# Kernel optimization log

Measured on AMD Instinct MI355X. Metric: run time of the kernel, lower is better.

The kernel has to match this reference:

```python
import jax, jax.numpy as jnp
import numpy as np

NX = 320   # image matrix (nRead)
NC = 8     # coils
NT = 8     # motion states
M = 65536  # non-Cartesian k-space samples per frame
OS = 2     # gridding oversampling factor


def setup_inputs() -> dict:
    key = jax.random.key(0)
    ks = jax.random.split(key, 7)
    kspace_r = jax.random.normal(ks[0], (NC, M), jnp.float32)
    kspace_i = jax.random.normal(ks[1], (NC, M), jnp.float32)
    # k-space trajectory normalized to [-0.5, 0.5)
    traj = jax.random.uniform(ks[2], (M, 2, NT), jnp.float32, -0.5, 0.5)
    csm_r = jax.random.normal(ks[3], (NC, NX, NX), jnp.float32)
    csm_i = jax.random.normal(ks[4], (NC, NX, NX), jnp.float32)
    dcf = jax.random.uniform(ks[5], (M, NT), jnp.float32)
    # motion/flow field in pixels, [NX, NX, 2, NT]
    motions = 3.0 * jax.random.normal(ks[6], (NX, NX, 2, NT), jnp.float32)
    return dict(kspace_r=kspace_r, kspace_i=kspace_i, traj=traj,
                csm_r=csm_r, csm_i=csm_i, dcf=dcf, motions=motions)


def _grid_adjoint(kspace, traj_t, dcf_t, csm):
    """Adjoint NUFFT (gpuNUFFT adj_op): density-compensated bilinear gridding
    onto a 2x oversampled Cartesian grid, inverse FFT, center crop,
    deapodization, and conjugate coil combination."""
    G = OS * NX
    data = (kspace * dcf_t[None, :]).astype(jnp.complex64)  # [NC, M]
    u = (traj_t[:, 0] + 0.5) * G
    v = (traj_t[:, 1] + 0.5) * G
    u0 = jnp.floor(u)
    v0 = jnp.floor(v)
    du = (u - u0).astype(jnp.float32)
    dv = (v - v0).astype(jnp.float32)
    i0 = u0.astype(jnp.int32) % G
    i1 = (i0 + 1) % G
    j0 = v0.astype(jnp.int32) % G
    j1 = (j0 + 1) % G
    grid = jnp.zeros((NC, G, G), jnp.complex64)
    grid = grid.at[:, i0, j0].add(data * ((1.0 - du) * (1.0 - dv)))
    grid = grid.at[:, i1, j0].add(data * (du * (1.0 - dv)))
    grid = grid.at[:, i0, j1].add(data * ((1.0 - du) * dv))
    grid = grid.at[:, i1, j1].add(data * (du * dv))
    im_os = jnp.fft.fftshift(
        jnp.fft.ifft2(jnp.fft.ifftshift(grid, axes=(-2, -1)), axes=(-2, -1)),
        axes=(-2, -1))
    s = (G - NX) // 2
    im = im_os[:, s:s + NX, s:s + NX]  # [NC, NX, NX]
    # deapodization: FT of the triangle (bilinear) gridding kernel is sinc^2
    x = (jnp.arange(NX, dtype=jnp.float32) - NX // 2) / G
    d = jnp.sinc(x) ** 2
    im = im / (d[:, None] * d[None, :])
    # conjugate coil combine with sensitivity maps
    return jnp.sum(jnp.conj(csm) * im, axis=0).astype(jnp.complex64)


def _bilinear_warp(im, flow):
    """apply_sparse_motion: sparse bilinear-interpolation warp of a 2D image
    by a per-pixel displacement field flow[..., 0:2] (in pixels)."""
    Nx, Ny = im.shape
    xs = jnp.arange(Nx, dtype=jnp.float32)[:, None] + flow[..., 0]
    ys = jnp.arange(Ny, dtype=jnp.float32)[None, :] + flow[..., 1]
    xs = jnp.clip(xs, 0.0, Nx - 1.0)
    ys = jnp.clip(ys, 0.0, Ny - 1.0)
    x0 = jnp.floor(xs).astype(jnp.int32)
    y0 = jnp.floor(ys).astype(jnp.int32)
    x1 = jnp.minimum(x0 + 1, Nx - 1)
    y1 = jnp.minimum(y0 + 1, Ny - 1)
    dx = xs - x0.astype(jnp.float32)
    dy = ys - y0.astype(jnp.float32)
    return ((1.0 - dx) * (1.0 - dy) * im[x0, y0]
            + dx * (1.0 - dy) * im[x1, y0]
            + (1.0 - dx) * dy * im[x0, y1]
            + dx * dy * im[x1, y1])


def reference(kspace_r, kspace_i, traj, csm_r, csm_i, dcf, motions):
    kspace = (kspace_r + 1j * kspace_i).astype(jnp.complex64)
    csm = (csm_r + 1j * csm_i).astype(jnp.complex64)

    def frame(traj_t, dcf_t, flow_t):
        im = _grid_adjoint(kspace, traj_t, dcf_t, csm)
        return _bilinear_warp(im, flow_t)

    # vmap over motion states: traj[..., t], dcf[..., t], motions[..., t]
    per_frame = jax.vmap(frame, in_axes=(2, 1, 3))(traj, dcf, motions)  # [NT, NX, NX]
    out = jnp.sum(per_frame, axis=0)  # temporal sum, complex [NX, NX]
    return jnp.stack([out.real, out.imag], axis=-1)  # [NX, NX, 2]
```

## Files before the change

### kernel.cpp

```cpp
#include <hip/hip_runtime.h>
#include <math.h>

#define NXI 320
#define NCI 8
#define NTI 8
#define MI  65536
#define GI  640
#define G2I (GI*GI)
#define NPIX (NXI*NXI)
#define REC_F 20
#define SP 642
#define NBINS (NTI*G2I)
#define SCAN_BLKS (NBINS/1024)

__device__ inline float2 cmul(float2 a, float2 b) {
    return make_float2(a.x*b.x - a.y*b.y, a.x*b.y + a.y*b.x);
}
__device__ inline float2 cadd(float2 a, float2 b) { return make_float2(a.x+b.x, a.y+b.y); }
__device__ inline float2 csub(float2 a, float2 b) { return make_float2(a.x-b.x, a.y-b.y); }

__device__ inline float2 shfl_xor_c(float2 v, int m) {
    return make_float2(__shfl_xor(v.x, m, 64), __shfl_xor(v.y, m, 64));
}

__device__ inline void cell_of(const float* __restrict__ traj, int m, int f,
                               int& i0s, int& j0s, float& du, float& dv)
{
    float tu = traj[(m*2 + 0)*NTI + f];
    float tv = traj[(m*2 + 1)*NTI + f];
    float u = (tu + 0.5f) * (float)GI;
    float v = (tv + 0.5f) * (float)GI;
    float fu = floorf(u), fv = floorf(v);
    du = u - fu; dv = v - fv;
    i0s = (int)fu + GI/2; if (i0s >= GI) i0s -= GI;
    j0s = (int)fv + GI/2; if (j0s >= GI) j0s -= GI;
}

__global__ __launch_bounds__(256) void count_cells(
    const float* __restrict__ traj, int* __restrict__ counts)
{
    int tid = blockIdx.x * 256 + threadIdx.x;
    int f = tid >> 16, m = tid & (MI - 1);
    int i0s, j0s; float du, dv;
    cell_of(traj, m, f, i0s, j0s, du, dv);
    atomicAdd(&counts[f*G2I + i0s*GI + j0s], 1);
}

__device__ inline int scan1024(int v, int tid, int* tmp) {
    tmp[tid] = v; __syncthreads();
    for (int d = 1; d < 1024; d <<= 1) {
        int y = (tid >= d) ? tmp[tid - d] : 0;
        __syncthreads();
        tmp[tid] += y;
        __syncthreads();
    }
    return tmp[tid];
}

__global__ __launch_bounds__(1024) void scanA(const int* __restrict__ counts,
                                              int* __restrict__ binstart,
                                              int* __restrict__ sums)
{
    __shared__ int tmp[1024];
    int tid = threadIdx.x;
    int i = blockIdx.x * 1024 + tid;
    int v = counts[i];
    int incl = scan1024(v, tid, tmp);
    binstart[i] = incl - v;
    if (tid == 1023) sums[blockIdx.x] = incl;
}

__global__ __launch_bounds__(1024) void scanB(int* __restrict__ sums)
{
    __shared__ int tmp[1024];
    int tid = threadIdx.x;
    int base = tid * 4;
    int v[4]; int s = 0;
    #pragma unroll
    for (int q = 0; q < 4; ++q) {
        int idx = base + q;
        v[q] = (idx < SCAN_BLKS) ? sums[idx] : 0;
        s += v[q];
    }
    int incl = scan1024(s, tid, tmp);
    int run = incl - s;
    #pragma unroll
    for (int q = 0; q < 4; ++q) {
        int idx = base + q;
        if (idx < SCAN_BLKS) sums[idx] = run;
        run += v[q];
    }
}

__global__ __launch_bounds__(1024) void scanC(int* __restrict__ binstart,
                                              const int* __restrict__ sums,
                                              int* __restrict__ cursor)
{
    int i = blockIdx.x * 1024 + threadIdx.x;
    int v = binstart[i] + sums[blockIdx.x];
    binstart[i] = v;
    cursor[i] = v;
    if (i == NBINS - 1) binstart[NBINS] = NTI * MI;
}

__global__ __launch_bounds__(256) void scatter_cells(
    const float* __restrict__ kr, const float* __restrict__ ki,
    const float* __restrict__ traj, const float* __restrict__ dcf,
    int* __restrict__ cursor, float* __restrict__ recs)
{
    int tid = blockIdx.x * 256 + threadIdx.x;
    int f = tid >> 16, m = tid & (MI - 1);
    int i0s, j0s; float du, dv;
    cell_of(traj, m, f, i0s, j0s, du, dv);
    float w = dcf[m*NTI + f];
    int slot = atomicAdd(&cursor[f*G2I + i0s*GI + j0s], 1);
    float4* r = (float4*)(recs + (size_t)slot * REC_F);
    r[0] = make_float4(du, dv, 0.f, 0.f);
    #pragma unroll
    for (int q = 0; q < 4; ++q) {
        int c0 = 2*q;
        r[1+q] = make_float4(kr[c0*MI + m]*w,     ki[c0*MI + m]*w,
                             kr[(c0+1)*MI + m]*w, ki[(c0+1)*MI + m]*w);
    }
}

__device__ inline void dft5p(float2 x0, float2 x1, float2 x2, float2 x3, float2 x4,
                             float2* X)
{
    const float c1 = 0.309016994f, c2 = -0.809016994f;
    const float s1 = 0.951056516f, s2 =  0.587785252f;
    float2 S1 = cadd(x1, x4), D1 = csub(x1, x4);
    float2 S2 = cadd(x2, x3), D2 = csub(x2, x3);
    X[0] = make_float2(x0.x + S1.x + S2.x, x0.y + S1.y + S2.y);
    float2 A = make_float2(x0.x + c1*S1.x + c2*S2.x, x0.y + c1*S1.y + c2*S2.y);
    float2 T = make_float2(s1*D1.x + s2*D2.x,        s1*D1.y + s2*D2.y);
    float2 B = make_float2(x0.x + c2*S1.x + c1*S2.x, x0.y + c2*S1.y + c1*S2.y);
    float2 U = make_float2(s2*D1.x - s1*D2.x,        s2*D1.y - s1*D2.y);
    X[1] = make_float2(A.x - T.y, A.y + T.x);
    X[4] = make_float2(A.x + T.y, A.y - T.x);
    X[2] = make_float2(B.x - U.y, B.y + U.x);
    X[3] = make_float2(B.x + U.y, B.y - U.x);
}

__device__ inline int fft640_reg(float2* a, int lane, float2* Z,
                                 const float2* __restrict__ T)
{
    const float PI = 3.14159265358979f;
    #pragma unroll
    for (int s = 0; s < 6; ++s) {
        const int h = 32 >> s;
        bool low = (lane & h) == 0;
        float2 wt = T[(lane << s) & 63];
        float2 w = low ? make_float2(1.f, 0.f) : wt;
        #pragma unroll
        for (int n = 0; n < 10; ++n) {
            float2 p = shfl_xor_c(a[n], h);
            float2 t = low ? cadd(p, a[n]) : csub(a[n], p);
            a[n] = cmul(t, w);
        }
    }
    int k1 = __brev(lane) >> 26;
    float th = (2.0f * PI / 640.0f) * (float)k1;
    float sn, cs;
    __sincosf(th, &sn, &cs);
    float2 wb = make_float2(cs, sn);
    float2 w = wb;
    #pragma unroll
    for (int n = 1; n < 10; ++n) {
        a[n] = cmul(a[n], w);
        w = cmul(w, wb);
    }
    float2 E[5], O[5];
    dft5p(a[0], a[2], a[4], a[6], a[8], E);
    dft5p(a[1], a[3], a[5], a[7], a[9], O);
    const float2 tk[5] = {{1.f, 0.f},
                          { 0.809016994f, 0.587785252f},
                          { 0.309016994f, 0.951056516f},
                          {-0.309016994f, 0.951056516f},
                          {-0.809016994f, 0.587785252f}};
    #pragma unroll
    for (int k = 0; k < 5; ++k) {
        float2 t = cmul(tk[k], O[k]);
        Z[k]     = cadd(E[k], t);
        Z[k + 5] = csub(E[k], t);
    }
    return k1;
}

__device__ inline void fill_T(float2* T, int tid, int nthr) {
    const float PI = 3.14159265358979f;
    for (int q = tid; q < 64; q += nthr) {
        float sn, cs;
        __sincosf((2.0f * PI / 64.0f) * q, &sn, &cs);
        T[q] = make_float2(cs, sn);
    }
}

__global__ __launch_bounds__(512) void row_fft(
    const int* __restrict__ binstart, const float* __restrict__ recs,
    float2* __restrict__ rowout)
{
    __shared__ float2 A[NCI][SP];
    __shared__ int boff[2][GI+1];
    __shared__ float2 T[64];
    int bid = blockIdx.x;
    int i = bid % GI;
    int f = bid / GI;
    int tid = threadIdx.x;
    fill_T(&T[0], tid, 512);
    int im1 = i ? i - 1 : GI - 1;
    const int base0 = f*G2I + i*GI;
    const int base1 = f*G2I + im1*GI;
    for (int k = tid; k <= GI; k += 512) {
        boff[0][k] = binstart[base0 + k];
        boff[1][k] = binstart[base1 + k];
    }
    __syncthreads();

    for (int j = tid; j < GI; j += 512) {
        int jm1 = j ? j - 1 : GI - 1;
        float2 acc[NCI];
        #pragma unroll
        for (int c = 0; c < NCI; ++c) acc[c] = make_float2(0.f, 0.f);
        #pragma unroll
        for (int p = 0; p < 2; ++p) {
            #pragma unroll
            for (int side = 0; side < 2; ++side) {
                int b = side ? jm1 : j;
                int s0 = boff[p][b], s1 = boff[p][b+1];
                for (int s = s0; s < s1; ++s) {
                    const float4* R = (const float4*)(recs + (size_t)s*REC_F);
                    float4 h4 = R[0];
                    float wr = p ? h4.x : (1.f - h4.x);
                    float w  = wr * (side ? h4.y : (1.f - h4.y));
                    float4 d0 = R[1], d1 = R[2], d2 = R[3], d3 = R[4];
                    acc[0].x += w*d0.x; acc[0].y += w*d0.y;
                    acc[1].x += w*d0.z; acc[1].y += w*d0.w;
                    acc[2].x += w*d1.x; acc[2].y += w*d1.y;
                    acc[3].x += w*d1.z; acc[3].y += w*d1.w;
                    acc[4].x += w*d2.x; acc[4].y += w*d2.y;
                    acc[5].x += w*d2.z; acc[5].y += w*d2.w;
                    acc[6].x += w*d3.x; acc[6].y += w*d3.y;
                    acc[7].x += w*d3.z; acc[7].y += w*d3.w;
                }
            }
        }
        #pragma unroll
        for (int c = 0; c < NCI; ++c) A[c][j] = acc[c];
    }
    __syncthreads();

    int wv = tid >> 6, lane = tid & 63;
    float2 a[10];
    #pragma unroll
    for (int n = 0; n < 10; ++n) a[n] = A[wv][10*lane + n];
    float2 Z[10];
    int k1 = fft640_reg(a, lane, Z, &T[0]);
    #pragma unroll
    for (int k2 = 0; k2 < 10; ++k2) {
        int yc = k1 + 64*k2 + 160; if (yc >= GI) yc -= GI;
        A[wv][yc] = Z[k2];
    }
    float2* dst = rowout + (((size_t)f*NCI + wv)*GI + i)*NXI;
    #pragma unroll
    for (int q = 0; q < 5; ++q) {
        int yc = lane + 64*q;
        dst[yc] = A[wv][yc];
    }
}

__global__ __launch_bounds__(512) void col_fft(
    const float2* __restrict__ rowout, float2* __restrict__ colimg)
{
    __shared__ float2 A[8][SP];
    __shared__ float2 T[64];
    int bid = blockIdx.x;
    int g = bid % 40;
    int c = (bid / 40) % NCI;
    int f = bid / (40*NCI);
    int y0 = g * 8;
    int tid = threadIdx.x;
    fill_T(&T[0], tid, 512);
    const float2* src = rowout + ((size_t)f*NCI + c)*GI*NXI + y0;
    for (int idx = tid; idx < 8*GI; idx += 512) {
        int l = idx & 7, k = idx >> 3;
        A[l][k] = src[(size_t)k*NXI + l];
    }
    __syncthreads();
    int wv = tid >> 6, lane = tid & 63;
    float2 a[10];
    #pragma unroll
    for (int n = 0; n < 10; ++n) a[n] = A[wv][10*lane + n];
    float2 Z[10];
    int k1 = fft640_reg(a, lane, Z, &T[0]);
    #pragma unroll
    for (int k2 = 0; k2 < 10; ++k2) {
        int xx = k1 + 64*k2 + 160; if (xx >= GI) xx -= GI;
        A[wv][xx] = Z[k2];
    }
    __syncthreads();
    float2* dst = colimg + ((size_t)f*NCI + c)*NPIX + y0;
    for (int idx = tid; idx < 8*NXI; idx += 512) {
        int l = idx & 7, xx = idx >> 3;
        dst[(size_t)xx*NXI + l] = A[l][xx];
    }
}

__global__ __launch_bounds__(256) void combine_kernel(
    const float2* __restrict__ colimg, const float* __restrict__ csr,
    const float* __restrict__ csi, float2* __restrict__ img)
{
    int f = blockIdx.y;
    int pix = blockIdx.x * 256 + threadIdx.x;
    int x = pix / NXI, y = pix - x*NXI;
    const float PI = 3.14159265358979f;
    float tx = (x - 160) * (1.0f/GI);
    float ty = (y - 160) * (1.0f/GI);
    float dx = 1.0f, dy = 1.0f;
    if (x != 160) { float s = __sinf(PI*tx) / (PI*tx); dx = s*s; }
    if (y != 160) { float s = __sinf(PI*ty) / (PI*ty); dy = s*s; }
    float scale = 1.0f / ((float)G2I * dx * dy);
    float accr = 0.f, acci = 0.f;
    #pragma unroll
    for (int c = 0; c < NCI; ++c) {
        float2 g = colimg[((size_t)f*NCI + c)*NPIX + pix];
        float cr = csr[c*NPIX + pix];
        float ci = csi[c*NPIX + pix];
        accr += cr*g.x + ci*g.y;
        acci += cr*g.y - ci*g.x;
    }
    img[(size_t)f*NPIX + pix] = make_float2(accr*scale, acci*scale);
}

__global__ __launch_bounds__(256) void warp_sum(
    const float2* __restrict__ img, const float* __restrict__ motions,
    float* __restrict__ out)
{
    int pix = blockIdx.x * 256 + threadIdx.x;
    int x = pix / NXI, y = pix - x*NXI;
    float accr = 0.f, acci = 0.f;
    #pragma unroll
    for (int f = 0; f < NTI; ++f) {
        float fx = motions[(size_t)(pix*2 + 0)*NTI + f];
        float fy = motions[(size_t)(pix*2 + 1)*NTI + f];
        float xs = fminf(fmaxf((float)x + fx, 0.0f), (float)(NXI-1));
        float ys = fminf(fmaxf((float)y + fy, 0.0f), (float)(NXI-1));
        int x0 = (int)floorf(xs);
        int y0 = (int)floorf(ys);
        int x1 = min(x0+1, NXI-1);
        int y1 = min(y0+1, NXI-1);
        float dx = xs - (float)x0;
        float dy = ys - (float)y0;
        const float2* im = img + (size_t)f*NPIX;
        float2 v00 = im[x0*NXI + y0];
        float2 v10 = im[x1*NXI + y0];
        float2 v01 = im[x0*NXI + y1];
        float2 v11 = im[x1*NXI + y1];
        float w00 = (1.f-dx)*(1.f-dy), w10 = dx*(1.f-dy);
        float w01 = (1.f-dx)*dy,       w11 = dx*dy;
        accr += w00*v00.x + w10*v10.x + w01*v01.x + w11*v11.x;
        acci += w00*v00.y + w10*v10.y + w01*v01.y + w11*v11.y;
    }
    out[pix*2+0] = accr;
    out[pix*2+1] = acci;
}

extern "C" void kernel_launch(void* const* d_in, const int* in_sizes, int n_in,
                              void* d_out, int out_size, void* d_ws, size_t ws_size,
                              hipStream_t stream)
{
    const float* kr   = (const float*)d_in[0];
    const float* ki   = (const float*)d_in[1];
    const float* traj = (const float*)d_in[2];
    const float* csr  = (const float*)d_in[3];
    const float* csi  = (const float*)d_in[4];
    const float* dcf  = (const float*)d_in[5];
    const float* mot  = (const float*)d_in[6];
    float* out = (float*)d_out;

    char* ws = (char*)d_ws;
    float*  recs     = (float*)ws;
    ws += (size_t)NTI * MI * REC_F * sizeof(float);
    float2* rowout   = (float2*)ws;
    ws += (size_t)NTI * NCI * GI * NXI * sizeof(float2);
    float2* colimg   = (float2*)ws;
    ws += (size_t)NTI * NCI * NPIX * sizeof(float2);
    float2* img      = (float2*)ws;
    ws += (size_t)NTI * NPIX * sizeof(float2);
    int*    counts   = (int*)ws;  ws += (size_t)NBINS * sizeof(int);
    int*    binstart = (int*)ws;  ws += ((size_t)NBINS + 16) * sizeof(int);
    int*    cursor   = (int*)ws;  ws += (size_t)NBINS * sizeof(int);
    int*    sums     = (int*)ws;  ws += (size_t)SCAN_BLKS * sizeof(int);

    hipMemsetAsync(counts, 0, (size_t)NBINS * sizeof(int), stream);
    count_cells  <<<NTI*MI/256, 256, 0, stream>>>(traj, counts);
    scanA        <<<SCAN_BLKS, 1024, 0, stream>>>(counts, binstart, sums);
    scanB        <<<1,         1024, 0, stream>>>(sums);
    scanC        <<<SCAN_BLKS, 1024, 0, stream>>>(binstart, sums, cursor);
    scatter_cells<<<NTI*MI/256, 256, 0, stream>>>(kr, ki, traj, dcf, cursor, recs);
    row_fft      <<<NTI*GI,     512, 0, stream>>>(binstart, recs, rowout);
    col_fft      <<<NTI*NCI*40, 512, 0, stream>>>(rowout, colimg);
    combine_kernel<<<dim3(NPIX/256, NTI), 256, 0, stream>>>(colimg, csr, csi, img);
    warp_sum     <<<NPIX/256,   256, 0, stream>>>(img, mot, out);
}
```

Baseline: 344.3 us.

## Vectorize complex math, prune FFT outputs, swizzle shared memory, merge gather loops

Rewrites the complex arithmetic with two-wide float vector types so the compiler can emit packed FP32 instructions. The 640-point FFT now computes and writes only the 320 cropped outputs and works out its twiddles with sincos instead of reading a shared table. The row gather reads bin offsets straight from global memory and walks two adjacent bins as one contiguous range. Column-FFT shared arrays use an XOR swizzle instead of padding to avoid bank conflicts, and launch bounds now request higher occupancy. The risks are extra transcendental instructions, uncached global reads of bin offsets, and register pressure under the tighter launch bounds.

```diff
diff --git a/kernel.cpp b/kernel.cpp
--- a/kernel.cpp
+++ b/kernel.cpp
@@ -9,18 +9,22 @@
 #define G2I (GI*GI)
 #define NPIX (NXI*NXI)
 #define REC_F 20
-#define SP 642
 #define NBINS (NTI*G2I)
 #define SCAN_BLKS (NBINS/1024)
 
-__device__ inline float2 cmul(float2 a, float2 b) {
-    return make_float2(a.x*b.x - a.y*b.y, a.x*b.y + a.y*b.x);
-}
-__device__ inline float2 cadd(float2 a, float2 b) { return make_float2(a.x+b.x, a.y+b.y); }
-__device__ inline float2 csub(float2 a, float2 b) { return make_float2(a.x-b.x, a.y-b.y); }
-
-__device__ inline float2 shfl_xor_c(float2 v, int m) {
-    return make_float2(__shfl_xor(v.x, m, 64), __shfl_xor(v.y, m, 64));
+typedef float v2f __attribute__((ext_vector_type(2)));
+
+__device__ inline v2f cmul(v2f a, v2f b) {
+    v2f axx = __builtin_shufflevector(a, a, 0, 0);
+    v2f ayy = __builtin_shufflevector(a, a, 1, 1);
+    v2f byx = __builtin_shufflevector(b, b, 1, 0);
+    v2f r = axx * b;
+    v2f t = ayy * byx;
+    return r + v2f{-t.x, t.y};
+}
+
+__device__ inline v2f shfl_xor_v(v2f v, int m) {
+    return v2f{__shfl_xor(v.x, m, 64), __shfl_xor(v.y, m, 64)};
 }
 
 __device__ inline void cell_of(const float* __restrict__ traj, int m, int f,
@@ -124,124 +128,123 @@
     }
 }
 
-__device__ inline void dft5p(float2 x0, float2 x1, float2 x2, float2 x3, float2 x4,
-                             float2* X)
+__device__ inline void dft5p(v2f x0, v2f x1, v2f x2, v2f x3, v2f x4, v2f* X)
 {
     const float c1 = 0.309016994f, c2 = -0.809016994f;
     const float s1 = 0.951056516f, s2 =  0.587785252f;
-    float2 S1 = cadd(x1, x4), D1 = csub(x1, x4);
-    float2 S2 = cadd(x2, x3), D2 = csub(x2, x3);
-    X[0] = make_float2(x0.x + S1.x + S2.x, x0.y + S1.y + S2.y);
-    float2 A = make_float2(x0.x + c1*S1.x + c2*S2.x, x0.y + c1*S1.y + c2*S2.y);
-    float2 T = make_float2(s1*D1.x + s2*D2.x,        s1*D1.y + s2*D2.y);
-    float2 B = make_float2(x0.x + c2*S1.x + c1*S2.x, x0.y + c2*S1.y + c1*S2.y);
-    float2 U = make_float2(s2*D1.x - s1*D2.x,        s2*D1.y - s1*D2.y);
-    X[1] = make_float2(A.x - T.y, A.y + T.x);
-    X[4] = make_float2(A.x + T.y, A.y - T.x);
-    X[2] = make_float2(B.x - U.y, B.y + U.x);
-    X[3] = make_float2(B.x + U.y, B.y - U.x);
-}
-
-__device__ inline int fft640_reg(float2* a, int lane, float2* Z,
-                                 const float2* __restrict__ T)
+    v2f S1 = x1 + x4, D1 = x1 - x4;
+    v2f S2 = x2 + x3, D2 = x2 - x3;
+    X[0] = x0 + S1 + S2;
+    v2f A = x0 + c1*S1 + c2*S2;
+    v2f T = s1*D1 + s2*D2;
+    v2f B = x0 + c2*S1 + c1*S2;
+    v2f U = s2*D1 - s1*D2;
+    v2f iT = v2f{-T.y, T.x};
+    v2f iU = v2f{-U.y, U.x};
+    X[1] = A + iT;  X[4] = A - iT;
+    X[2] = B + iU;  X[3] = B - iU;
+}
+
+__device__ inline void fft640_pruned(v2f* a, int lane, v2f* line, int xorm)
 {
     const float PI = 3.14159265358979f;
     #pragma unroll
     for (int s = 0; s < 6; ++s) {
         const int h = 32 >> s;
         bool low = (lane & h) == 0;
-        float2 wt = T[(lane << s) & 63];
-        float2 w = low ? make_float2(1.f, 0.f) : wt;
+        int k = (lane << s) & 63;
+        float sn, cs;
+        __sincosf((2.0f * PI / 64.0f) * (float)k, &sn, &cs);
+        v2f ws = v2f{cs, sn};
         #pragma unroll
         for (int n = 0; n < 10; ++n) {
-            float2 p = shfl_xor_c(a[n], h);
-            float2 t = low ? cadd(p, a[n]) : csub(a[n], p);
-            a[n] = cmul(t, w);
+            v2f p = shfl_xor_v(a[n], h);
+            v2f tl = p + a[n];
+            v2f th = cmul(a[n] - p, ws);
+            a[n] = low ? tl : th;
         }
     }
     int k1 = __brev(lane) >> 26;
-    float th = (2.0f * PI / 640.0f) * (float)k1;
+    float th2 = (2.0f * PI / 640.0f) * (float)k1;
     float sn, cs;
-    __sincosf(th, &sn, &cs);
-    float2 wb = make_float2(cs, sn);
-    float2 w = wb;
+    __sincosf(th2, &sn, &cs);
+    v2f wb = v2f{cs, sn};
+    v2f w = wb;
     #pragma unroll
     for (int n = 1; n < 10; ++n) {
         a[n] = cmul(a[n], w);
         w = cmul(w, wb);
     }
-    float2 E[5], O[5];
+    v2f E[5], O[5];
     dft5p(a[0], a[2], a[4], a[6], a[8], E);
     dft5p(a[1], a[3], a[5], a[7], a[9], O);
-    const float2 tk[5] = {{1.f, 0.f},
-                          { 0.809016994f, 0.587785252f},
-                          { 0.309016994f, 0.951056516f},
-                          {-0.309016994f, 0.951056516f},
-                          {-0.809016994f, 0.587785252f}};
-    #pragma unroll
-    for (int k = 0; k < 5; ++k) {
-        float2 t = cmul(tk[k], O[k]);
-        Z[k]     = cadd(E[k], t);
-        Z[k + 5] = csub(E[k], t);
-    }
-    return k1;
-}
-
-__device__ inline void fill_T(float2* T, int tid, int nthr) {
-    const float PI = 3.14159265358979f;
-    for (int q = tid; q < 64; q += nthr) {
-        float sn, cs;
-        __sincosf((2.0f * PI / 64.0f) * q, &sn, &cs);
-        T[q] = make_float2(cs, sn);
-    }
-}
-
-__global__ __launch_bounds__(512) void row_fft(
+    const v2f tk1 = { 0.809016994f, 0.587785252f};
+    const v2f tk2 = { 0.309016994f, 0.951056516f};
+    const v2f tk3 = {-0.309016994f, 0.951056516f};
+    const v2f tk4 = {-0.809016994f, 0.587785252f};
+    v2f t1 = cmul(tk1, O[1]);
+    v2f t2 = cmul(tk2, O[2]);
+    v2f t3 = cmul(tk3, O[3]);
+    v2f t4 = cmul(tk4, O[4]);
+    bool hi = (k1 >= 32);
+    line[(160 + k1) ^ xorm] = E[0] + O[0];
+    line[(224 + k1) ^ xorm] = E[1] + t1;
+    int yx = hi ? (k1 - 32) : (288 + k1);
+    v2f zx = hi ? (E[2] - t2) : (E[2] + t2);
+    line[yx ^ xorm] = zx;
+    line[(32 + k1) ^ xorm] = E[3] - t3;
+    line[(96 + k1) ^ xorm] = E[4] - t4;
+}
+
+__global__ __launch_bounds__(512, 8) void row_fft(
     const int* __restrict__ binstart, const float* __restrict__ recs,
-    float2* __restrict__ rowout)
-{
-    __shared__ float2 A[NCI][SP];
-    __shared__ int boff[2][GI+1];
-    __shared__ float2 T[64];
+    v2f* __restrict__ rowout)
+{
+    __shared__ v2f A[NCI][GI];
     int bid = blockIdx.x;
     int i = bid % GI;
     int f = bid / GI;
     int tid = threadIdx.x;
-    fill_T(&T[0], tid, 512);
     int im1 = i ? i - 1 : GI - 1;
-    const int base0 = f*G2I + i*GI;
-    const int base1 = f*G2I + im1*GI;
-    for (int k = tid; k <= GI; k += 512) {
-        boff[0][k] = binstart[base0 + k];
-        boff[1][k] = binstart[base1 + k];
-    }
-    __syncthreads();
+    const int* bsr[2] = { binstart + f*G2I + i*GI,
+                          binstart + f*G2I + im1*GI };
 
     for (int j = tid; j < GI; j += 512) {
-        int jm1 = j ? j - 1 : GI - 1;
-        float2 acc[NCI];
+        v2f acc[NCI];
         #pragma unroll
-        for (int c = 0; c < NCI; ++c) acc[c] = make_float2(0.f, 0.f);
+        for (int c = 0; c < NCI; ++c) acc[c] = v2f{0.f, 0.f};
         #pragma unroll
         for (int p = 0; p < 2; ++p) {
-            #pragma unroll
-            for (int side = 0; side < 2; ++side) {
-                int b = side ? jm1 : j;
-                int s0 = boff[p][b], s1 = boff[p][b+1];
-                for (int s = s0; s < s1; ++s) {
+            const int* bs = bsr[p];
+            if (j > 0) {
+                int lo = bs[j-1], mid = bs[j], hi = bs[j+1];
+                for (int s = lo; s < hi; ++s) {
                     const float4* R = (const float4*)(recs + (size_t)s*REC_F);
                     float4 h4 = R[0];
                     float wr = p ? h4.x : (1.f - h4.x);
-                    float w  = wr * (side ? h4.y : (1.f - h4.y));
+                    float w  = wr * ((s < mid) ? h4.y : (1.f - h4.y));
                     float4 d0 = R[1], d1 = R[2], d2 = R[3], d3 = R[4];
-                    acc[0].x += w*d0.x; acc[0].y += w*d0.y;
-                    acc[1].x += w*d0.z; acc[1].y += w*d0.w;
-                    acc[2].x += w*d1.x; acc[2].y += w*d1.y;
-                    acc[3].x += w*d1.z; acc[3].y += w*d1.w;
-                    acc[4].x += w*d2.x; acc[4].y += w*d2.y;
-                    acc[5].x += w*d2.z; acc[5].y += w*d2.w;
-                    acc[6].x += w*d3.x; acc[6].y += w*d3.y;
-                    acc[7].x += w*d3.z; acc[7].y += w*d3.w;
+                    acc[0] += w * v2f{d0.x, d0.y};  acc[1] += w * v2f{d0.z, d0.w};
+                    acc[2] += w * v2f{d1.x, d1.y};  acc[3] += w * v2f{d1.z, d1.w};
+                    acc[4] += w * v2f{d2.x, d2.y};  acc[5] += w * v2f{d2.z, d2.w};
+                    acc[6] += w * v2f{d3.x, d3.y};  acc[7] += w * v2f{d3.z, d3.w};
+                }
+            } else {
+                #pragma unroll
+                for (int side = 0; side < 2; ++side) {
+                    int b = side ? 0 : (GI - 1);
+                    int s0 = bs[b], s1 = bs[b+1];
+                    for (int s = s0; s < s1; ++s) {
+                        const float4* R = (const float4*)(recs + (size_t)s*REC_F);
+                        float4 h4 = R[0];
+                        float wr = p ? h4.x : (1.f - h4.x);
+                        float w  = wr * (side ? (1.f - h4.y) : h4.y);
+                        float4 d0 = R[1], d1 = R[2], d2 = R[3], d3 = R[4];
+                        acc[0] += w * v2f{d0.x, d0.y};  acc[1] += w * v2f{d0.z, d0.w};
+                        acc[2] += w * v2f{d1.x, d1.y};  acc[3] += w * v2f{d1.z, d1.w};
+                        acc[4] += w * v2f{d2.x, d2.y};  acc[5] += w * v2f{d2.z, d2.w};
+                        acc[6] += w * v2f{d3.x, d3.y};  acc[7] += w * v2f{d3.z, d3.w};
+                    }
                 }
             }
         }
@@ -251,17 +254,11 @@
     __syncthreads();
 
     int wv = tid >> 6, lane = tid & 63;
-    float2 a[10];
+    v2f a[10];
     #pragma unroll
     for (int n = 0; n < 10; ++n) a[n] = A[wv][10*lane + n];
-    float2 Z[10];
-    int k1 = fft640_reg(a, lane, Z, &T[0]);
-    #pragma unroll
-    for (int k2 = 0; k2 < 10; ++k2) {
-        int yc = k1 + 64*k2 + 160; if (yc >= GI) yc -= GI;
-        A[wv][yc] = Z[k2];
-    }
-    float2* dst = rowout + (((size_t)f*NCI + wv)*GI + i)*NXI;
+    fft640_pruned(a, lane, A[wv], 0);
+    v2f* dst = rowout + (((size_t)f*NCI + wv)*GI + i)*NXI;
     #pragma unroll
     for (int q = 0; q < 5; ++q) {
         int yc = lane + 64*q;
@@ -269,40 +266,33 @@
     }
 }
 
-__global__ __launch_bounds__(512) void col_fft(
-    const float2* __restrict__ rowout, float2* __restrict__ colimg)
-{
-    __shared__ float2 A[8][SP];
-    __shared__ float2 T[64];
+__global__ __launch_bounds__(512, 8) void col_fft(
+    const v2f* __restrict__ rowout, v2f* __restrict__ colimg)
+{
+    __shared__ v2f A[8][GI];
     int bid = blockIdx.x;
     int g = bid % 40;
     int c = (bid / 40) % NCI;
     int f = bid / (40*NCI);
     int y0 = g * 8;
     int tid = threadIdx.x;
-    fill_T(&T[0], tid, 512);
-    const float2* src = rowout + ((size_t)f*NCI + c)*GI*NXI + y0;
+    const v2f* src = rowout + ((size_t)f*NCI + c)*GI*NXI + y0;
     for (int idx = tid; idx < 8*GI; idx += 512) {
         int l = idx & 7, k = idx >> 3;
-        A[l][k] = src[(size_t)k*NXI + l];
+        A[l][k ^ (4*(l & 3))] = src[(size_t)k*NXI + l];
     }
     __syncthreads();
     int wv = tid >> 6, lane = tid & 63;
-    float2 a[10];
-    #pragma unroll
-    for (int n = 0; n < 10; ++n) a[n] = A[wv][10*lane + n];
-    float2 Z[10];
-    int k1 = fft640_reg(a, lane, Z, &T[0]);
-    #pragma unroll
-    for (int k2 = 0; k2 < 10; ++k2) {
-        int xx = k1 + 64*k2 + 160; if (xx >= GI) xx -= GI;
-        A[wv][xx] = Z[k2];
-    }
+    int xm = 4 * (wv & 3);
+    v2f a[10];
+    #pragma unroll
+    for (int n = 0; n < 10; ++n) a[n] = A[wv][(10*lane + n) ^ xm];
+    fft640_pruned(a, lane, A[wv], xm);
     __syncthreads();
-    float2* dst = colimg + ((size_t)f*NCI + c)*NPIX + y0;
+    v2f* dst = colimg + ((size_t)f*NCI + c)*NPIX + y0;
     for (int idx = tid; idx < 8*NXI; idx += 512) {
         int l = idx & 7, xx = idx >> 3;
-        dst[(size_t)xx*NXI + l] = A[l][xx];
+        dst[(size_t)xx*NXI + l] = A[l][xx ^ (4*(l & 3))];
     }
 }
 
@@ -381,7 +371,7 @@
     char* ws = (char*)d_ws;
     float*  recs     = (float*)ws;
     ws += (size_t)NTI * MI * REC_F * sizeof(float);
-    float2* rowout   = (float2*)ws;
+    v2f*    rowout   = (v2f*)ws;
     ws += (size_t)NTI * NCI * GI * NXI * sizeof(float2);
     float2* colimg   = (float2*)ws;
     ws += (size_t)NTI * NCI * NPIX * sizeof(float2);
@@ -399,7 +389,7 @@
     scanC        <<<SCAN_BLKS, 1024, 0, stream>>>(binstart, sums, cursor);
     scatter_cells<<<NTI*MI/256, 256, 0, stream>>>(kr, ki, traj, dcf, cursor, recs);
     row_fft      <<<NTI*GI,     512, 0, stream>>>(binstart, recs, rowout);
-    col_fft      <<<NTI*NCI*40, 512, 0, stream>>>(rowout, colimg);
+    col_fft      <<<NTI*NCI*40, 512, 0, stream>>>(rowout, (v2f*)colimg);
     combine_kernel<<<dim3(NPIX/256, NTI), 256, 0, stream>>>(colimg, csr, csi, img);
     warp_sum     <<<NPIX/256,   256, 0, stream>>>(img, mot, out);
 }
```

New measurement: 306.9 us. 1.12x faster.
